# Optimization experiments

Measured on AMD Instinct MI355X. Metric: run time of the kernel, lower is better.

The kernel has to match this reference:

```python
import jax, jax.numpy as jnp
import numpy as np

N = 100000
E = 1600000
NEG_SLOPE = 0.2
DEPTH = 5


def setup_inputs() -> dict:
    key = jax.random.key(0)
    ks = jax.random.split(key, 8)
    x = jax.random.normal(ks[0], (N, 100), dtype=jnp.float32)
    edge_index = jax.random.randint(ks[1], (2, E), 0, N, dtype=jnp.int64)
    # layer 0: 100 -> 48; layers 1..4: 48 -> 48
    W0 = jax.random.normal(ks[2], (100, 48), dtype=jnp.float32) * 0.1
    Wrest = jax.random.normal(ks[3], (DEPTH - 1, 48, 48), dtype=jnp.float32) * 0.1
    a_src = jax.random.normal(ks[4], (DEPTH, 48), dtype=jnp.float32) * 0.1
    a_dst = jax.random.normal(ks[5], (DEPTH, 48), dtype=jnp.float32) * 0.1
    bias = jax.random.normal(ks[6], (DEPTH, 48), dtype=jnp.float32) * 0.1
    return {"x": x, "edge_index": edge_index, "W0": W0, "Wrest": Wrest,
            "a_src": a_src, "a_dst": a_dst, "bias": bias}


def _gat_layer(x, src, dst, W, a_s, a_d, b):
    h = x @ W                                   # [N, F]
    alpha_s = h @ a_s                           # [N]
    alpha_d = h @ a_d                           # [N]
    e = alpha_s[src] + alpha_d[dst]             # [E']
    e = jax.nn.leaky_relu(e, NEG_SLOPE)
    # segment softmax over edges grouped by destination node
    m = jax.ops.segment_max(e, dst, num_segments=N)
    m = jnp.where(jnp.isfinite(m), m, 0.0)      # empty segments -> 0
    p = jnp.exp(e - m[dst])
    s = jax.ops.segment_sum(p, dst, num_segments=N)
    alpha = p / jnp.maximum(s[dst], 1e-16)      # [E']
    out = jax.ops.segment_sum(alpha[:, None] * h[src], dst, num_segments=N)
    return out + b


def reference(x, edge_index, W0, Wrest, a_src, a_dst, bias):
    # PyG GATConv default add_self_loops=True
    loops = jnp.arange(N, dtype=edge_index.dtype)
    src = jnp.concatenate([edge_index[0], loops])
    dst = jnp.concatenate([edge_index[1], loops])
    Ws = [W0] + [Wrest[i] for i in range(DEPTH - 1)]
    h = x
    for l in range(DEPTH):
        h = _gat_layer(h, src, dst, Ws[l], a_src[l], a_dst[l], bias[l])
        h = jax.nn.elu(h)
    return h
```

## Files before the change

kernel.cpp:

```cpp
#include <hip/hip_runtime.h>

#define NN 100000
#define EE 1600000
#define ETOT (EE + NN)
#define FF 48
#define NEG 0.2f
#define BSH 9
#define BNODES 512
#define NBUK ((NN + BNODES - 1) / BNODES)
#define TILE 2048
#define G0BLK ((NN + 127) / 128)
#define HISTBLK 512
#define HROW 64

__device__ __forceinline__ unsigned short f2bf(float x) {
    unsigned u = __float_as_uint(x);
    u += 0x7FFF + ((u >> 16) & 1);
    return (unsigned short)(u >> 16);
}
__device__ __forceinline__ float bf2f(unsigned short b) {
    return __uint_as_float(((unsigned)b) << 16);
}
__device__ __forceinline__ unsigned pk(unsigned short a, unsigned short b) {
    return (unsigned)a | ((unsigned)b << 16);
}


template <int K, int KC, int R>
__device__ __forceinline__ void gemm_body(int bid, float* Wl, float* asl, float* adl,
                                          const float* __restrict__ in,
                                          const float* __restrict__ W,
                                          const float* __restrict__ a_s,
                                          const float* __restrict__ a_d,
                                          unsigned short* __restrict__ h16,
                                          float* __restrict__ as_,
                                          float* __restrict__ ad_) {
    int t = threadIdx.x;
    for (int i = t; i < K * FF / 4; i += 256)
        ((float4*)Wl)[i] = ((const float4*)W)[i];
    if (t < FF) { asl[t] = a_s[t]; adl[t] = a_d[t]; }
    __syncthreads();

    int fg = t & 3;
    int pr = t >> 2;
    int r0 = bid * (64 * R) + pr * R;
    if (r0 >= NN) return;

    constexpr int NC = K / KC;
    constexpr int QC = KC / 4;
    const float4* x4 = (const float4*)in;
    const float4* wl4 = (const float4*)Wl;

    float acc[R][12];
#pragma unroll
    for (int r = 0; r < R; r++)
#pragma unroll
        for (int j = 0; j < 12; j++) acc[r][j] = 0.f;

    for (int c = 0; c < NC; c++) {
        float xs[R][KC];
#pragma unroll
        for (int r = 0; r < R; r++) {
#pragma unroll
            for (int q = 0; q < QC; q++) {
                float4 v = x4[(size_t)(r0 + r) * (K / 4) + c * QC + q];
                xs[r][4 * q + 0] = v.x; xs[r][4 * q + 1] = v.y;
                xs[r][4 * q + 2] = v.z; xs[r][4 * q + 3] = v.w;
            }
        }
#pragma unroll
        for (int kk = 0; kk < KC; kk++) {
            const int k = c * KC + kk;
            const float4 w0 = wl4[k * 12 + fg * 3 + 0];
            const float4 w1 = wl4[k * 12 + fg * 3 + 1];
            const float4 w2 = wl4[k * 12 + fg * 3 + 2];
#pragma unroll
            for (int r = 0; r < R; r++) {
                const float xv = xs[r][kk];
                acc[r][0] = fmaf(xv, w0.x, acc[r][0]);
                acc[r][1] = fmaf(xv, w0.y, acc[r][1]);
                acc[r][2] = fmaf(xv, w0.z, acc[r][2]);
                acc[r][3] = fmaf(xv, w0.w, acc[r][3]);
                acc[r][4] = fmaf(xv, w1.x, acc[r][4]);
                acc[r][5] = fmaf(xv, w1.y, acc[r][5]);
                acc[r][6] = fmaf(xv, w1.z, acc[r][6]);
                acc[r][7] = fmaf(xv, w1.w, acc[r][7]);
                acc[r][8] = fmaf(xv, w2.x, acc[r][8]);
                acc[r][9] = fmaf(xv, w2.y, acc[r][9]);
                acc[r][10] = fmaf(xv, w2.z, acc[r][10]);
                acc[r][11] = fmaf(xv, w2.w, acc[r][11]);
            }
        }
    }

#pragma unroll
    for (int r = 0; r < R; r++) {
        uint2* hp = (uint2*)(h16 + (size_t)(r0 + r) * HROW + fg * 12);
        hp[0] = make_uint2(pk(f2bf(acc[r][0]), f2bf(acc[r][1])),
                           pk(f2bf(acc[r][2]), f2bf(acc[r][3])));
        hp[1] = make_uint2(pk(f2bf(acc[r][4]), f2bf(acc[r][5])),
                           pk(f2bf(acc[r][6]), f2bf(acc[r][7])));
        hp[2] = make_uint2(pk(f2bf(acc[r][8]), f2bf(acc[r][9])),
                           pk(f2bf(acc[r][10]), f2bf(acc[r][11])));
    }

    float ps[R], pd[R];
#pragma unroll
    for (int r = 0; r < R; r++) { ps[r] = 0.f; pd[r] = 0.f; }
#pragma unroll
    for (int j = 0; j < 12; j++) {
        float av = asl[fg * 12 + j], dv = adl[fg * 12 + j];
#pragma unroll
        for (int r = 0; r < R; r++) {
            ps[r] = fmaf(acc[r][j], av, ps[r]);
            pd[r] = fmaf(acc[r][j], dv, pd[r]);
        }
    }
#pragma unroll
    for (int r = 0; r < R; r++) {
        ps[r] += __shfl_xor(ps[r], 1); ps[r] += __shfl_xor(ps[r], 2);
        pd[r] += __shfl_xor(pd[r], 1); pd[r] += __shfl_xor(pd[r], 2);
    }
    if (fg == 0) {
#pragma unroll
        for (int r = 0; r < R; r++) {
            as_[r0 + r] = ps[r];
            ad_[r0 + r] = pd[r];
        }
    }
}

__global__ __launch_bounds__(256) void k_g0_hist(const float* __restrict__ x,
                                                 const float* __restrict__ W0,
                                                 const float* __restrict__ a_s,
                                                 const float* __restrict__ a_d,
                                                 unsigned short* __restrict__ h16,
                                                 float* __restrict__ as_,
                                                 float* __restrict__ ad_,
                                                 const int* __restrict__ ei,
                                                 int* __restrict__ bcnt) {
    __shared__ __align__(16) char smem[(100 * FF + 2 * FF) * 4];
    if (blockIdx.x < G0BLK) {
        float* Wl = (float*)smem;
        float* asl = Wl + 100 * FF;
        float* adl = asl + FF;
        gemm_body<100, 20, 2>(blockIdx.x, Wl, asl, adl, x, W0, a_s, a_d, h16, as_, ad_);
    } else {
        int* hh = (int*)smem;
        int t = threadIdx.x;
        int bid = blockIdx.x - G0BLK;
        hh[t] = 0;
        __syncthreads();
        for (int i = bid * 256 + t; i < ETOT; i += HISTBLK * 256) {
            int dd = (i < EE) ? ei[EE + i] : (i - EE);
            atomicAdd(&hh[dd >> BSH], 1);
        }
        __syncthreads();
        if (hh[t] > 0) atomicAdd(&bcnt[t], hh[t]);
    }
}

__global__ __launch_bounds__(256) void k_bscatter(const int* __restrict__ ei,
                                                  const int* __restrict__ bcnt,
                                                  int* __restrict__ bpos,
                                                  int2* __restrict__ pairs) {
    __shared__ int hist[256], incl[256], exc[256], curv[256], gb[256], sb[256];
    __shared__ int2 stage[TILE];
    __shared__ int staddr[TILE];
    int t = threadIdx.x;
    int bv = (t < NBUK) ? bcnt[t] : 0;
    sb[t] = bv;
    __syncthreads();
    for (int o = 1; o < 256; o <<= 1) {
        int x = (t >= o) ? sb[t - o] : 0;
        __syncthreads();
        sb[t] += x;
        __syncthreads();
    }
    int bexcl = sb[t] - bv;
    hist[t] = 0;
    __syncthreads();
    int base = blockIdx.x * TILE;
    int s[8], d[8], b[8];
#pragma unroll
    for (int j = 0; j < 8; j++) {
        int i = base + t + j * 256;
        if (i < ETOT) {
            int ss, dd;
            if (i < EE) { ss = ei[i]; dd = ei[EE + i]; }
            else { ss = i - EE; dd = ss; }
            s[j] = ss; d[j] = dd; b[j] = dd >> BSH;
            atomicAdd(&hist[b[j]], 1);
        } else {
            b[j] = -1;
        }
    }
    __syncthreads();
    int hv = hist[t];
    incl[t] = hv;
    __syncthreads();
    for (int o = 1; o < 256; o <<= 1) {
        int x = (t >= o) ? incl[t - o] : 0;
        __syncthreads();
        incl[t] += x;
        __syncthreads();
    }
    int excl = incl[t] - hv;
    exc[t] = excl;
    curv[t] = excl;
    if (hv > 0) gb[t] = bexcl + atomicAdd(&bpos[t], hv);
    __syncthreads();
    int total = incl[255];
#pragma unroll
    for (int j = 0; j < 8; j++) {
        if (b[j] >= 0) {
            int pos = atomicAdd(&curv[b[j]], 1);
            stage[pos] = make_int2(s[j], d[j]);
            staddr[pos] = gb[b[j]] + (pos - exc[b[j]]);
        }
    }
    __syncthreads();
    for (int i = t; i < total; i += 256) pairs[staddr[i]] = stage[i];
}

__global__ __launch_bounds__(512) void k_bfill(const int2* __restrict__ pairs,
                                               const int* __restrict__ bcnt,
                                               int* __restrict__ off,
                                               int* __restrict__ ssrc) {
    __shared__ int cnt[BNODES], cu[BNODES], sb[512];
    int blk = blockIdx.x;
    int t = threadIdx.x;
    int n0 = blk << BSH;
    int bv = (t < NBUK) ? bcnt[t] : 0;
    sb[t] = bv;
    __syncthreads();
    for (int o = 1; o < 512; o <<= 1) {
        int x = (t >= o) ? sb[t - o] : 0;
        __syncthreads();
        sb[t] += x;
        __syncthreads();
    }
    int beg = sb[blk] - bcnt[blk];
    int end = sb[blk];
    __syncthreads();
    cnt[t] = 0;
    __syncthreads();
    for (int i = beg + t; i < end; i += 512) {
        atomicAdd(&cnt[pairs[i].y - n0], 1);
    }
    __syncthreads();
    int v = cnt[t];
    sb[t] = v;
    __syncthreads();
    for (int o = 1; o < 512; o <<= 1) {
        int x = (t >= o) ? sb[t - o] : 0;
        __syncthreads();
        sb[t] += x;
        __syncthreads();
    }
    int excl = sb[t] - v;
    cu[t] = excl;
    if (n0 + t < NN) off[n0 + t] = beg + excl;
    if (blk == 0 && t == 0) off[NN] = ETOT;
    __syncthreads();
    for (int i = beg + t; i < end; i += 512) {
        int2 pr = pairs[i];
        int pos = atomicAdd(&cu[pr.y - n0], 1);
        ssrc[beg + pos] = pr.x;
    }
}

template <int K, int KC, int R>
__global__ __launch_bounds__(256) void k_gemm(const float* __restrict__ in,
                                              const float* __restrict__ W,
                                              const float* __restrict__ a_s,
                                              const float* __restrict__ a_d,
                                              unsigned short* __restrict__ h16,
                                              float* __restrict__ as_,
                                              float* __restrict__ ad_) {
    __shared__ float Wl[K * FF];
    __shared__ float asl[FF], adl[FF];
    gemm_body<K, KC, R>(blockIdx.x, Wl, asl, adl, in, W, a_s, a_d, h16, as_, ad_);
}


__global__ __launch_bounds__(256) void k_aggr(const unsigned short* __restrict__ h16,
                                              const float* __restrict__ as_,
                                              const float* __restrict__ ad_,
                                              const int* __restrict__ off,
                                              const int* __restrict__ ssrc,
                                              const float* __restrict__ bias,
                                              float* __restrict__ out) {
    int wave = threadIdx.x >> 6;
    int lane = threadIdx.x & 63;
    int d = blockIdx.x * 4 + wave;
    if (d >= NN) return;
    int beg = __builtin_amdgcn_readfirstlane(off[d]);
    int end = __builtin_amdgcn_readfirstlane(off[d + 1]);
    int deg = end - beg;
    float add = ad_[d];
    int fW = (lane < FF) ? lane : lane - FF;
    unsigned foff = (unsigned)(fW * 2);
    const char* hb = (const char*)h16;

    float acc = 0.f, s = 0.f;

    if (deg <= 64) {
        int srcb = 0;
        float e = -1e30f;
        if (lane < deg) {
            int src = ssrc[beg + lane];
            srcb = src << 7;
            float t = as_[src] + add;
            e = (t > 0.f) ? t : NEG * t;
        }
        float m = e;
#pragma unroll
        for (int o = 32; o; o >>= 1) m = fmaxf(m, __shfl_xor(m, o));
        float p = (lane < deg) ? __expf(e - m) : 0.f;
        float sv = p;
#pragma unroll
        for (int o = 32; o; o >>= 1) sv += __shfl_xor(sv, o);
        s = sv;

        unsigned pbits = __float_as_uint(p);
        int degR = (deg + 7) & ~7;
        for (int i = 0; i < degR; i += 8) {
            float pj[8], hv[8];
#pragma unroll
            for (int j = 0; j < 8; j++) {
                pj[j] = __uint_as_float(
                    (unsigned)__builtin_amdgcn_readlane((int)pbits, i + j));
                int sbj = __builtin_amdgcn_readlane(srcb, i + j);
                hv[j] = bf2f(*(const unsigned short*)(hb + (unsigned)sbj + foff));
            }
#pragma unroll
            for (int j = 0; j < 8; j++) acc = fmaf(pj[j], hv[j], acc);
        }
    } else {
        float m = -1e30f;
        for (int i = beg + lane; i < end; i += 64) {
            float t = as_[ssrc[i]] + add;
            t = (t > 0.f) ? t : NEG * t;
            m = fmaxf(m, t);
        }
#pragma unroll
        for (int o = 32; o; o >>= 1) m = fmaxf(m, __shfl_xor(m, o));
        for (int i = beg; i < end; i++) {
            int src = ssrc[i];
            float e = as_[src] + add;
            e = (e > 0.f) ? e : NEG * e;
            float pp = __expf(e - m);
            s += pp;
            if (lane < FF) acc = fmaf(pp, bf2f(h16[(size_t)src * HROW + lane]), acc);
        }
    }

    if (lane < FF) {
        float v = acc / fmaxf(s, 1e-16f) + bias[lane];
        v = (v > 0.f) ? v : (__expf(v) - 1.0f);
        out[(size_t)d * FF + lane] = v;
    }
}


static inline size_t alup(size_t x) { return (x + 255) & ~(size_t)255; }

extern "C" void kernel_launch(void* const* d_in, const int* in_sizes, int n_in,
                              void* d_out, int out_size, void* d_ws, size_t ws_size,
                              hipStream_t stream) {
    const float* x = (const float*)d_in[0];
    const int* ei = (const int*)d_in[1];
    const float* W0 = (const float*)d_in[2];
    const float* Wr = (const float*)d_in[3];
    const float* As = (const float*)d_in[4];
    const float* Ad = (const float*)d_in[5];
    const float* B = (const float*)d_in[6];
    float* out = (float*)d_out;

    char* p = (char*)d_ws;
    int* off = (int*)p;      p += alup((NN + 1) * sizeof(int));
    int* bcnt = (int*)p;     p += 1024;
    int* bpos = (int*)p;     p += 1024;
    int2* pairs = (int2*)p;  p += alup((size_t)ETOT * sizeof(int2));
    int* ssrc = (int*)p;     p += alup((size_t)ETOT * sizeof(int) + 256);
    unsigned short* h16 = (unsigned short*)p;
    p += alup((size_t)NN * HROW * sizeof(unsigned short) + 256);
    float* act = (float*)p;  p += alup((size_t)NN * FF * sizeof(float) + 256);
    float* as_ = (float*)p;  p += alup(NN * sizeof(float));
    float* ad_ = (float*)p;  p += alup(NN * sizeof(float));

    hipMemsetAsync(bcnt, 0, 2048, stream);
    k_g0_hist<<<G0BLK + HISTBLK, 256, 0, stream>>>(x, W0, As, Ad, h16, as_, ad_, ei, bcnt);
    k_bscatter<<<(ETOT + TILE - 1) / TILE, 256, 0, stream>>>(ei, bcnt, bpos, pairs);
    k_bfill<<<NBUK, 512, 0, stream>>>(pairs, bcnt, off, ssrc);

    for (int l = 0; l < 5; l++) {
        if (l > 0) {
            int g = (NN + 255) / 256;
            k_gemm<48, 16, 4><<<g, 256, 0, stream>>>(act, Wr + (size_t)(l - 1) * 48 * 48,
                                                     As + l * 48, Ad + l * 48, h16, as_, ad_);
        }
        k_aggr<<<(NN + 3) / 4, 256, 0, stream>>>(h16, as_, ad_, off, ssrc, B + l * 48,
                                                 (l == 4) ? out : act);
    }
}
```

Baseline: 411.7 us.

## Store intermediate activations in bf16 and load gather indices per edge

Intermediate layer activations are now written by the aggregation kernel as bf16 rather than fp32, and the 48-wide GEMM reads them with 16-byte bf16 loads that it unpacks to fp32. This halves activation write and read traffic between layers, at the cost of extra rounding error. The aggregation inner loop also changes: each lane now reloads the source index from ssrc in memory for every edge instead of broadcasting it from a register with readlane. That adds memory loads to the gather loop.

After: 449.6 us. 1.09x slower.

```diff
diff --git a/kernel.cpp b/kernel.cpp
--- a/kernel.cpp
+++ b/kernel.cpp
@@ -21,14 +21,20 @@
 __device__ __forceinline__ float bf2f(unsigned short b) {
     return __uint_as_float(((unsigned)b) << 16);
 }
+__device__ __forceinline__ float bflo(unsigned u) {
+    return __uint_as_float(u << 16);
+}
+__device__ __forceinline__ float bfhi(unsigned u) {
+    return __uint_as_float(u & 0xffff0000u);
+}
 __device__ __forceinline__ unsigned pk(unsigned short a, unsigned short b) {
     return (unsigned)a | ((unsigned)b << 16);
 }
 
 
-template <int K, int KC, int R>
+template <int K, int KC, int R, bool IN16>
 __device__ __forceinline__ void gemm_body(int bid, float* Wl, float* asl, float* adl,
-                                          const float* __restrict__ in,
+                                          const void* __restrict__ inp,
                                           const float* __restrict__ W,
                                           const float* __restrict__ a_s,
                                           const float* __restrict__ a_d,
@@ -48,7 +54,6 @@
 
     constexpr int NC = K / KC;
     constexpr int QC = KC / 4;
-    const float4* x4 = (const float4*)in;
     const float4* wl4 = (const float4*)Wl;
 
     float acc[R][12];
@@ -59,13 +64,29 @@
 
     for (int c = 0; c < NC; c++) {
         float xs[R][KC];
-#pragma unroll
-        for (int r = 0; r < R; r++) {
-#pragma unroll
-            for (int q = 0; q < QC; q++) {
-                float4 v = x4[(size_t)(r0 + r) * (K / 4) + c * QC + q];
-                xs[r][4 * q + 0] = v.x; xs[r][4 * q + 1] = v.y;
-                xs[r][4 * q + 2] = v.z; xs[r][4 * q + 3] = v.w;
+        if (IN16) {
+            const unsigned short* a16 = (const unsigned short*)inp;
+#pragma unroll
+            for (int r = 0; r < R; r++) {
+#pragma unroll
+                for (int q = 0; q < KC / 8; q++) {
+                    uint4 u = *(const uint4*)(a16 + (size_t)(r0 + r) * K + c * KC + q * 8);
+                    xs[r][8 * q + 0] = bflo(u.x); xs[r][8 * q + 1] = bfhi(u.x);
+                    xs[r][8 * q + 2] = bflo(u.y); xs[r][8 * q + 3] = bfhi(u.y);
+                    xs[r][8 * q + 4] = bflo(u.z); xs[r][8 * q + 5] = bfhi(u.z);
+                    xs[r][8 * q + 6] = bflo(u.w); xs[r][8 * q + 7] = bfhi(u.w);
+                }
+            }
+        } else {
+            const float4* x4 = (const float4*)inp;
+#pragma unroll
+            for (int r = 0; r < R; r++) {
+#pragma unroll
+                for (int q = 0; q < QC; q++) {
+                    float4 v = x4[(size_t)(r0 + r) * (K / 4) + c * QC + q];
+                    xs[r][4 * q + 0] = v.x; xs[r][4 * q + 1] = v.y;
+                    xs[r][4 * q + 2] = v.z; xs[r][4 * q + 3] = v.w;
+                }
             }
         }
 #pragma unroll
@@ -144,7 +165,8 @@
         float* Wl = (float*)smem;
         float* asl = Wl + 100 * FF;
         float* adl = asl + FF;
-        gemm_body<100, 20, 2>(blockIdx.x, Wl, asl, adl, x, W0, a_s, a_d, h16, as_, ad_);
+        gemm_body<100, 20, 2, false>(blockIdx.x, Wl, asl, adl, x, W0, a_s, a_d,
+                                     h16, as_, ad_);
     } else {
         int* hh = (int*)smem;
         int t = threadIdx.x;
@@ -270,27 +292,29 @@
     }
 }
 
-template <int K, int KC, int R>
-__global__ __launch_bounds__(256) void k_gemm(const float* __restrict__ in,
-                                              const float* __restrict__ W,
-                                              const float* __restrict__ a_s,
-                                              const float* __restrict__ a_d,
-                                              unsigned short* __restrict__ h16,
-                                              float* __restrict__ as_,
-                                              float* __restrict__ ad_) {
-    __shared__ float Wl[K * FF];
+__global__ __launch_bounds__(256) void k_gemm48(const unsigned short* __restrict__ a16,
+                                                const float* __restrict__ W,
+                                                const float* __restrict__ a_s,
+                                                const float* __restrict__ a_d,
+                                                unsigned short* __restrict__ h16,
+                                                float* __restrict__ as_,
+                                                float* __restrict__ ad_) {
+    __shared__ float Wl[48 * FF];
     __shared__ float asl[FF], adl[FF];
-    gemm_body<K, KC, R>(blockIdx.x, Wl, asl, adl, in, W, a_s, a_d, h16, as_, ad_);
-}
-
-
+    gemm_body<48, 16, 4, true>(blockIdx.x, Wl, asl, adl, a16, W, a_s, a_d,
+                               h16, as_, ad_);
+}
+
+
+template <bool LAST>
 __global__ __launch_bounds__(256) void k_aggr(const unsigned short* __restrict__ h16,
                                               const float* __restrict__ as_,
                                               const float* __restrict__ ad_,
                                               const int* __restrict__ off,
                                               const int* __restrict__ ssrc,
                                               const float* __restrict__ bias,
-                                              float* __restrict__ out) {
+                                              float* __restrict__ out,
+                                              unsigned short* __restrict__ act16) {
     int wave = threadIdx.x >> 6;
     int lane = threadIdx.x & 63;
     int d = blockIdx.x * 4 + wave;
@@ -300,17 +324,13 @@
     int deg = end - beg;
     float add = ad_[d];
     int fW = (lane < FF) ? lane : lane - FF;
-    unsigned foff = (unsigned)(fW * 2);
-    const char* hb = (const char*)h16;
 
     float acc = 0.f, s = 0.f;
 
     if (deg <= 64) {
-        int srcb = 0;
         float e = -1e30f;
         if (lane < deg) {
             int src = ssrc[beg + lane];
-            srcb = src << 7;
             float t = as_[src] + add;
             e = (t > 0.f) ? t : NEG * t;
         }
@@ -329,10 +349,12 @@
             float pj[8], hv[8];
 #pragma unroll
             for (int j = 0; j < 8; j++) {
+                int src_j = (i + j < deg) ? ssrc[beg + i + j] : 0;
+                const unsigned short* hrow =
+                    h16 + ((size_t)(unsigned)src_j << 6);
                 pj[j] = __uint_as_float(
                     (unsigned)__builtin_amdgcn_readlane((int)pbits, i + j));
-                int sbj = __builtin_amdgcn_readlane(srcb, i + j);
-                hv[j] = bf2f(*(const unsigned short*)(hb + (unsigned)sbj + foff));
+                hv[j] = bf2f(hrow[fW]);
             }
 #pragma unroll
             for (int j = 0; j < 8; j++) acc = fmaf(pj[j], hv[j], acc);
@@ -359,7 +381,10 @@
     if (lane < FF) {
         float v = acc / fmaxf(s, 1e-16f) + bias[lane];
         v = (v > 0.f) ? v : (__expf(v) - 1.0f);
-        out[(size_t)d * FF + lane] = v;
+        if (LAST)
+            out[(size_t)d * FF + lane] = v;
+        else
+            act16[(size_t)d * FF + lane] = f2bf(v);
     }
 }
 
@@ -386,7 +411,8 @@
     int* ssrc = (int*)p;     p += alup((size_t)ETOT * sizeof(int) + 256);
     unsigned short* h16 = (unsigned short*)p;
     p += alup((size_t)NN * HROW * sizeof(unsigned short) + 256);
-    float* act = (float*)p;  p += alup((size_t)NN * FF * sizeof(float) + 256);
+    unsigned short* act16 = (unsigned short*)p;
+    p += alup((size_t)NN * FF * sizeof(unsigned short) + 256);
     float* as_ = (float*)p;  p += alup(NN * sizeof(float));
     float* ad_ = (float*)p;  p += alup(NN * sizeof(float));
 
@@ -398,10 +424,14 @@
     for (int l = 0; l < 5; l++) {
         if (l > 0) {
             int g = (NN + 255) / 256;
-            k_gemm<48, 16, 4><<<g, 256, 0, stream>>>(act, Wr + (size_t)(l - 1) * 48 * 48,
-                                                     As + l * 48, Ad + l * 48, h16, as_, ad_);
-        }
-        k_aggr<<<(NN + 3) / 4, 256, 0, stream>>>(h16, as_, ad_, off, ssrc, B + l * 48,
-                                                 (l == 4) ? out : act);
-    }
-}
+            k_gemm48<<<g, 256, 0, stream>>>(act16, Wr + (size_t)(l - 1) * 48 * 48,
+                                            As + l * 48, Ad + l * 48, h16, as_, ad_);
+        }
+        if (l == 4)
+            k_aggr<true><<<(NN + 3) / 4, 256, 0, stream>>>(h16, as_, ad_, off, ssrc,
+                                                           B + l * 48, out, nullptr);
+        else
+            k_aggr<false><<<(NN + 3) / 4, 256, 0, stream>>>(h16, as_, ad_, off, ssrc,
+                                                            B + l * 48, nullptr, act16);
+    }
+}
```
